# Performance work log

Hardware: AMD Instinct MI355X
Metric: run time of the kernel (lower is better)

## Reference

```python
import jax, jax.numpy as jnp
import numpy as np

SEQ, NSTEPS = 8192, 2048
IDIM, HDIM, NL = 256, 1024, 4


def setup_inputs() -> dict:
    key = jax.random.key(0)
    ks = jax.random.split(key, 6)
    s = 0.02  # small init so tanh recurrence stays well-conditioned
    return {
        "xs": jax.random.normal(ks[0], (SEQ, IDIM), dtype=jnp.float32),
        "Wx0": jax.random.normal(ks[1], (IDIM, HDIM), dtype=jnp.float32) * s,
        "Wh0": jax.random.normal(ks[2], (HDIM, HDIM), dtype=jnp.float32) * s,
        "b0": jnp.zeros((HDIM,), dtype=jnp.float32),
        "Wx_rest": jax.random.normal(ks[3], (NL - 1, HDIM, HDIM), dtype=jnp.float32) * s,
        "Wh_rest": jax.random.normal(ks[4], (NL - 1, HDIM, HDIM), dtype=jnp.float32) * s,
        "b_rest": jnp.zeros((NL - 1, HDIM), dtype=jnp.float32),
        "out_W": jax.random.normal(ks[5], (IDIM, HDIM), dtype=jnp.float32) * s,  # eqx Linear: (out, in)
        "out_b": jnp.zeros((IDIM,), dtype=jnp.float32),
        "n_steps": NSTEPS,
    }


def _layer_scan(xs, Wx, Wh, b):
    # open-loop scan of one tanh RNN cell over the whole sequence
    pre = xs @ Wx + b  # (T, H): hoist input projection out of the scan

    def step(h, p):
        h = jnp.tanh(p + h @ Wh)
        return h, h

    h0 = jnp.zeros((Wh.shape[0],), dtype=xs.dtype)
    last, outs = jax.lax.scan(step, h0, pre)
    return last, outs


def reference(xs, Wx0, Wh0, b0, Wx_rest, Wh_rest, b_rest, out_W, out_b, n_steps):
    # open_loop: run each layer's scan over the full sequence
    states = []
    h, seq = _layer_scan(xs, Wx0, Wh0, b0)
    states.append(h)
    for i in range(Wx_rest.shape[0]):
        h, seq = _layer_scan(seq, Wx_rest[i], Wh_rest[i], b_rest[i])
        states.append(h)
    ol_outs = seq @ out_W.T + out_b  # (T, IDIM) vmap'd out_layer

    def ar_step(carry, _):
        sts, x = carry
        new_sts = []
        h = jnp.tanh(x @ Wx0 + sts[0] @ Wh0 + b0)
        new_sts.append(h)
        x = h
        for i in range(Wx_rest.shape[0]):
            h = jnp.tanh(x @ Wx_rest[i] + sts[i + 1] @ Wh_rest[i] + b_rest[i])
            new_sts.append(h)
            x = h
        x = out_W @ x + out_b
        return (tuple(new_sts), x), x

    carry = (tuple(states), ol_outs[-1])
    _, ar_outs = jax.lax.scan(ar_step, carry, None, length=n_steps)
    return jnp.concatenate([ol_outs, ar_outs], axis=0)  # (T + n_steps, IDIM)
```

## Files before the change

kernel.cpp:

```cpp
#include <hip/hip_runtime.h>
#include <math.h>

#define SEQ    8192
#define NSTEPS 2048
#define NTOT   (SEQ + NSTEPS)
#define IDIM   256
#define HDIM   1024

#define NWG    128
#define TPB    512
#define WPB    8
#define RD     8

typedef unsigned long long u64;

#define WT_FLOATS   (8ull*HDIM*HDIM)
#define BF_FLOAT    WT_FLOATS
#define RING_FLOAT  (WT_FLOATS + HDIM)
#define RING_U64S   (4ull*RD*HDIM)
#define PROG_FLOAT  (RING_FLOAT + 2ull*RING_U64S)


__global__ void k_fuse_w(const float* __restrict__ outW, const float* __restrict__ Wx0,
                         float* __restrict__ ws) {
    int l = blockIdx.x * 256 + threadIdx.x;
    int j = blockIdx.y;
    float acc = 0.f;
    for (int k = 0; k < IDIM; ++k)
        acc += outW[(size_t)k * HDIM + l] * Wx0[(size_t)k * HDIM + j];
    ws[(size_t)j * HDIM + l] = acc;
}

__global__ void k_fuse_b(const float* __restrict__ b0, const float* __restrict__ outb,
                         const float* __restrict__ Wx0, float* __restrict__ ws) {
    int j = blockIdx.x * 256 + threadIdx.x;
    float acc = b0[j];
    for (int k = 0; k < IDIM; ++k)
        acc += outb[k] * Wx0[(size_t)k * HDIM + j];
    ws[BF_FLOAT + j] = acc;
}

__global__ void k_pack(const float* __restrict__ Wh0, const float* __restrict__ Wxr,
                       const float* __restrict__ Whr, float* __restrict__ ws) {
    __shared__ float t[32][33];
    int z = blockIdx.z;
    const float* src; int slot;
    if (z == 0)      { src = Wh0;                                  slot = 1; }
    else if (z <= 3) { src = Wxr + (size_t)(z - 1) * HDIM * HDIM;  slot = 2 * z; }
    else             { src = Whr + (size_t)(z - 4) * HDIM * HDIM;  slot = 2 * (z - 4) + 3; }
    int j0 = blockIdx.x * 32, l0 = blockIdx.y * 32;
    t[threadIdx.y][threadIdx.x] = src[(size_t)(l0 + threadIdx.y) * HDIM + j0 + threadIdx.x];
    __syncthreads();
    float* dst = ws + (size_t)slot * HDIM * HDIM;
    dst[(size_t)(j0 + threadIdx.y) * HDIM + (l0 + threadIdx.x)] = t[threadIdx.x][threadIdx.y];
}

__global__ void k_init(float* __restrict__ ws) {
    int t = blockIdx.x * blockDim.x + threadIdx.x;
    ((u64*)(ws + RING_FLOAT))[t] = 0ull;
    if (t < NWG) ((unsigned*)(ws + PROG_FLOAT))[t] = 0u;
}


__device__ __forceinline__ float wsum(float v) {
#pragma unroll
    for (int off = 32; off > 0; off >>= 1) v += __shfl_xor(v, off, 64);
    return v;
}

__device__ __forceinline__ float ftanh(float x) {
    x = fminf(15.f, fmaxf(-15.f, x));
    float e = __builtin_amdgcn_exp2f(x * 2.8853900817779268f);
    return (e - 1.f) * __builtin_amdgcn_rcpf(e + 1.f);
}

__device__ __forceinline__ void capture8(const u64* slot, unsigned want,
                                         float* dst, int lane, int kbase) {
    unsigned done = 0;
    for (;;) {
        u64 v[8];
#pragma unroll
        for (int k = 0; k < 8; ++k) {
            v[k] = 0;
            if (!(done & (1u << k)))
                v[k] = __hip_atomic_load(slot + lane + 64 * (kbase + k),
                                         __ATOMIC_RELAXED, __HIP_MEMORY_SCOPE_AGENT);
        }
#pragma unroll
        for (int k = 0; k < 8; ++k) {
            if (!(done & (1u << k)) && ((unsigned)(v[k] >> 32) == want)) {
                dst[lane + 64 * (kbase + k)] = __uint_as_float((unsigned)v[k]);
                done |= 1u << k;
            }
        }
        if (__all(done == 0xFFu)) return;
    }
}

__global__ __launch_bounds__(TPB, 1) void k_scan(
    const float* __restrict__ xs, const float* __restrict__ Wx0,
    const float* __restrict__ b0, const float* __restrict__ brest,
    const float* __restrict__ outW, const float* __restrict__ outb,
    float* __restrict__ ws, float* __restrict__ out)
{
    const int lane  = threadIdx.x & 63;
    const int wv    = threadIdx.x >> 6;
    const int layer = blockIdx.x >> 5;
    const int wgl   = blockIdx.x & 31;
    const int jw    = wgl * WPB + wv;
    const int j0    = jw * 4;

    __shared__ float ldsOwn[2][HDIM];
    __shared__ float ldsUp[2][HDIM];

    u64* ring = (u64*)(ws + RING_FLOAT);
    unsigned* prog = (unsigned*)(ws + PROG_FLOAT);
    const int cons = (layer + 1) & 3;

    float A[4][16], B[4][16];
#pragma unroll
    for (int c = 0; c < 4; ++c)
#pragma unroll
        for (int k = 0; k < 16; ++k) {
            A[c][k] = ws[((size_t)(2 * layer) * HDIM + (j0 + c)) * HDIM + lane + 64 * k];
            B[c][k] = ws[((size_t)(2 * layer + 1) * HDIM + (j0 + c)) * HDIM + lane + 64 * k];
        }
    float wx0[4][4];
    if (layer == 0) {
#pragma unroll
        for (int c = 0; c < 4; ++c)
#pragma unroll
            for (int k = 0; k < 4; ++k)
                wx0[c][k] = Wx0[(size_t)(lane + 64 * k) * HDIM + (j0 + c)];
    }
    float ow[16]; float obv = 0.f;
    if (layer == 3) {
#pragma unroll
        for (int k = 0; k < 16; ++k) ow[k] = outW[(size_t)jw * HDIM + lane + 64 * k];
        obv = outb[jw];
    }
    float bb[4], bfc[4];
#pragma unroll
    for (int c = 0; c < 4; ++c) {
        bb[c]  = (layer == 0) ? b0[j0 + c] : brest[(size_t)(layer - 1) * HDIM + j0 + c];
        bfc[c] = (layer == 0) ? ws[BF_FLOAT + j0 + c] : 0.f;
    }

    int minp = 0;

    for (int n = 1; n <= NTOT; ++n) {
        const int par = n & 1;
        const bool xphase = (layer == 0) && (n <= SEQ);

        if (minp < n - 7) {
            for (;;) {
                unsigned pv = __hip_atomic_load(&prog[cons * 32 + (lane & 31)],
                                                __ATOMIC_RELAXED, __HIP_MEMORY_SCOPE_AGENT);
#pragma unroll
                for (int off = 32; off > 0; off >>= 1) {
                    unsigned o = (unsigned)__shfl_xor((int)pv, off, 64);
                    pv = pv < o ? pv : o;
                }
                minp = (int)pv;
                if (minp >= n - 7) break;
                __builtin_amdgcn_s_sleep(2);
            }
        }

        float xv[4];
        if (xphase) {
            const float* xr = xs + (size_t)(n - 1) * IDIM;
#pragma unroll
            for (int k = 0; k < 4; ++k) xv[k] = xr[lane + 64 * k];
        }

        if (wv < 2) {
            capture8(ring + ((size_t)layer * RD + ((n - 1) & (RD - 1))) * HDIM,
                     (unsigned)(n - 1), ldsOwn[par], lane, wv * 8);
        } else if (wv < 4 && !xphase) {
            const int ul = (layer == 0) ? 3 : layer - 1;
            const unsigned want = (layer == 0) ? (unsigned)(n - 1) : (unsigned)n;
            capture8(ring + ((size_t)ul * RD + (want & (RD - 1))) * HDIM,
                     want, ldsUp[par], lane, (wv - 2) * 8);
        }
        __syncthreads();
        if (threadIdx.x == 0)
            __hip_atomic_store(&prog[blockIdx.x], (unsigned)n, __ATOMIC_RELAXED, __HIP_MEMORY_SCOPE_AGENT);

        float a0 = 0.f, a1 = 0.f, a2 = 0.f, a3 = 0.f;
        if (xphase) {
#pragma unroll
            for (int k = 0; k < 4; ++k) {
                float x = xv[k];
                a0 += x * wx0[0][k]; a1 += x * wx0[1][k]; a2 += x * wx0[2][k]; a3 += x * wx0[3][k];
            }
        } else {
#pragma unroll
            for (int k = 0; k < 16; ++k) {
                float x = ldsUp[par][lane + 64 * k];
                a0 += x * A[0][k]; a1 += x * A[1][k]; a2 += x * A[2][k]; a3 += x * A[3][k];
            }
        }
#pragma unroll
        for (int k = 0; k < 16; ++k) {
            float y = ldsOwn[par][lane + 64 * k];
            a0 += y * B[0][k]; a1 += y * B[1][k]; a2 += y * B[2][k]; a3 += y * B[3][k];
        }
        a0 = wsum(a0); a1 = wsum(a1); a2 = wsum(a2); a3 = wsum(a3);
        const bool fph = (layer == 0) && (n > SEQ);
        float r0 = ftanh(a0 + (fph ? bfc[0] : bb[0]));
        float r1 = ftanh(a1 + (fph ? bfc[1] : bb[1]));
        float r2 = ftanh(a2 + (fph ? bfc[2] : bb[2]));
        float r3 = ftanh(a3 + (fph ? bfc[3] : bb[3]));

        {
            u64* dst = ring + ((size_t)layer * RD + (n & (RD - 1))) * HDIM + j0;
            if (lane < 4) {
                float v = (lane == 0) ? r0 : (lane == 1) ? r1 : (lane == 2) ? r2 : r3;
                __hip_atomic_store(dst + lane,
                                   ((u64)(unsigned)n << 32) | (u64)__float_as_uint(v),
                                   __ATOMIC_RELAXED, __HIP_MEMORY_SCOPE_AGENT);
            }
        }

        if (layer == 3 && n >= 2) {
            float a = 0.f;
#pragma unroll
            for (int k = 0; k < 16; ++k) a += ldsOwn[par][lane + 64 * k] * ow[k];
            a = wsum(a);
            if (lane == 0) out[(size_t)(n - 2) * IDIM + jw] = a + obv;
        }
    }

    if (layer == 3) {
        if (wv < 2)
            capture8(ring + ((size_t)3 * RD + (NTOT & (RD - 1))) * HDIM,
                     (unsigned)NTOT, ldsOwn[0], lane, wv * 8);
        __syncthreads();
        float a = 0.f;
#pragma unroll
        for (int k = 0; k < 16; ++k) a += ldsOwn[0][lane + 64 * k] * ow[k];
        a = wsum(a);
        if (lane == 0) out[(size_t)(NTOT - 1) * IDIM + jw] = a + obv;
    }
}


extern "C" void kernel_launch(void* const* d_in, const int* in_sizes, int n_in,
                              void* d_out, int out_size, void* d_ws, size_t ws_size,
                              hipStream_t stream) {
    (void)in_sizes; (void)n_in; (void)out_size; (void)ws_size;
    const float* xs   = (const float*)d_in[0];
    const float* Wx0  = (const float*)d_in[1];
    const float* Wh0  = (const float*)d_in[2];
    const float* b0   = (const float*)d_in[3];
    const float* Wxr  = (const float*)d_in[4];
    const float* Whr  = (const float*)d_in[5];
    const float* brst = (const float*)d_in[6];
    const float* outW = (const float*)d_in[7];
    const float* outb = (const float*)d_in[8];
    float* ws  = (float*)d_ws;
    float* out = (float*)d_out;

    k_fuse_w<<<dim3(4, HDIM), dim3(256), 0, stream>>>(outW, Wx0, ws);
    k_fuse_b<<<dim3(4), dim3(256), 0, stream>>>(b0, outb, Wx0, ws);
    k_pack<<<dim3(32, 32, 7), dim3(32, 32), 0, stream>>>(Wh0, Wxr, Whr, ws);
    k_init<<<dim3(64), dim3(512), 0, stream>>>(ws);

    void* args[] = { (void*)&xs, (void*)&Wx0, (void*)&b0, (void*)&brst,
                     (void*)&outW, (void*)&outb, (void*)&ws, (void*)&out };
    hipError_t e = hipLaunchCooperativeKernel((void*)k_scan, dim3(NWG), dim3(TPB),
                                              args, 0, stream);
    if (e != hipSuccess) {
        k_scan<<<dim3(NWG), dim3(TPB), 0, stream>>>(xs, Wx0, b0, brst, outW, outb, ws, out);
    }
}
```

Measured before the change: 50.00 ms.

## Co-locate each layer's workgroups on one XCD and poll a local-cache ring first

```diff
diff --git a/kernel.cpp b/kernel.cpp
--- a/kernel.cpp
+++ b/kernel.cpp
@@ -7,18 +7,18 @@
 #define IDIM   256
 #define HDIM   1024
 
-#define NWG    128
+#define NWG    256
 #define TPB    512
-#define WPB    8
 #define RD     8
 
 typedef unsigned long long u64;
 
 #define WT_FLOATS   (8ull*HDIM*HDIM)
 #define BF_FLOAT    WT_FLOATS
-#define RING_FLOAT  (WT_FLOATS + HDIM)
-#define RING_U64S   (4ull*RD*HDIM)
-#define PROG_FLOAT  (RING_FLOAT + 2ull*RING_U64S)
+
+__device__ u64 g_llring[4ull * RD * HDIM];
+__device__ u64 g_lring [4ull * RD * HDIM];
+__device__ unsigned g_prog[128];
 
 
 __global__ void k_fuse_w(const float* __restrict__ outW, const float* __restrict__ Wx0,
@@ -55,10 +55,9 @@
     dst[(size_t)(j0 + threadIdx.y) * HDIM + (l0 + threadIdx.x)] = t[threadIdx.x][threadIdx.y];
 }
 
-__global__ void k_init(float* __restrict__ ws) {
-    int t = blockIdx.x * blockDim.x + threadIdx.x;
-    ((u64*)(ws + RING_FLOAT))[t] = 0ull;
-    if (t < NWG) ((unsigned*)(ws + PROG_FLOAT))[t] = 0u;
+__global__ void k_init() {
+    int t = threadIdx.x;
+    if (t < 128) g_prog[t] = 0u;
 }
 
 
@@ -74,27 +73,49 @@
     return (e - 1.f) * __builtin_amdgcn_rcpf(e + 1.f);
 }
 
-__device__ __forceinline__ void capture8(const u64* slot, unsigned want,
-                                         float* dst, int lane, int kbase) {
+__device__ __forceinline__ void ld4_sc0(const u64* p0, const u64* p1,
+                                        const u64* p2, const u64* p3,
+                                        u64& v0, u64& v1, u64& v2, u64& v3) {
+    asm volatile("global_load_dwordx2 %0, %4, off sc0\n\t"
+                 "global_load_dwordx2 %1, %5, off sc0\n\t"
+                 "global_load_dwordx2 %2, %6, off sc0\n\t"
+                 "global_load_dwordx2 %3, %7, off sc0\n\t"
+                 "s_waitcnt vmcnt(0)"
+                 : "=&v"(v0), "=&v"(v1), "=&v"(v2), "=&v"(v3)
+                 : "v"(p0), "v"(p1), "v"(p2), "v"(p3)
+                 : "memory");
+}
+
+__device__ __forceinline__ int cap4_ad(const u64* lb, const u64* gb, unsigned want,
+                                       float* dst, int lane, int kb, int budget) {
+    const int i0 = lane + 64 * (kb + 0), i1 = lane + 64 * (kb + 1);
+    const int i2 = lane + 64 * (kb + 2), i3 = lane + 64 * (kb + 3);
     unsigned done = 0;
+    for (int it = 0; it < budget; ++it) {
+        u64 v0, v1, v2, v3;
+        ld4_sc0(lb + i0, lb + i1, lb + i2, lb + i3, v0, v1, v2, v3);
+        if (!(done & 1u) && (unsigned)(v0 >> 32) == want) { dst[i0] = __uint_as_float((unsigned)v0); done |= 1u; }
+        if (!(done & 2u) && (unsigned)(v1 >> 32) == want) { dst[i1] = __uint_as_float((unsigned)v1); done |= 2u; }
+        if (!(done & 4u) && (unsigned)(v2 >> 32) == want) { dst[i2] = __uint_as_float((unsigned)v2); done |= 4u; }
+        if (!(done & 8u) && (unsigned)(v3 >> 32) == want) { dst[i3] = __uint_as_float((unsigned)v3); done |= 8u; }
+        if (__all(done == 0xFu)) return 1;
+    }
     for (;;) {
-        u64 v[8];
-#pragma unroll
-        for (int k = 0; k < 8; ++k) {
-            v[k] = 0;
-            if (!(done & (1u << k)))
-                v[k] = __hip_atomic_load(slot + lane + 64 * (kbase + k),
-                                         __ATOMIC_RELAXED, __HIP_MEMORY_SCOPE_AGENT);
-        }
-#pragma unroll
-        for (int k = 0; k < 8; ++k) {
-            if (!(done & (1u << k)) && ((unsigned)(v[k] >> 32) == want)) {
-                dst[lane + 64 * (kbase + k)] = __uint_as_float((unsigned)v[k]);
-                done |= 1u << k;
-            }
-        }
-        if (__all(done == 0xFFu)) return;
-    }
+        u64 v0 = __hip_atomic_load(gb + i0, __ATOMIC_RELAXED, __HIP_MEMORY_SCOPE_AGENT);
+        u64 v1 = __hip_atomic_load(gb + i1, __ATOMIC_RELAXED, __HIP_MEMORY_SCOPE_AGENT);
+        u64 v2 = __hip_atomic_load(gb + i2, __ATOMIC_RELAXED, __HIP_MEMORY_SCOPE_AGENT);
+        u64 v3 = __hip_atomic_load(gb + i3, __ATOMIC_RELAXED, __HIP_MEMORY_SCOPE_AGENT);
+        if (!(done & 1u) && (unsigned)(v0 >> 32) == want) { dst[i0] = __uint_as_float((unsigned)v0); done |= 1u; }
+        if (!(done & 2u) && (unsigned)(v1 >> 32) == want) { dst[i1] = __uint_as_float((unsigned)v1); done |= 2u; }
+        if (!(done & 4u) && (unsigned)(v2 >> 32) == want) { dst[i2] = __uint_as_float((unsigned)v2); done |= 4u; }
+        if (!(done & 8u) && (unsigned)(v3 >> 32) == want) { dst[i3] = __uint_as_float((unsigned)v3); done |= 8u; }
+        if (__all(done == 0xFu)) return 0;
+    }
+}
+
+__device__ __forceinline__ void cap4_llc(const u64* gb, unsigned want,
+                                         float* dst, int lane, int kb) {
+    cap4_ad((const u64*)0, gb, want, dst, lane, kb, 0);
 }
 
 __global__ __launch_bounds__(TPB, 1) void k_scan(
@@ -103,19 +124,21 @@
     const float* __restrict__ outW, const float* __restrict__ outb,
     float* __restrict__ ws, float* __restrict__ out)
 {
+    const int res = blockIdx.x & 7;
+    if (res >= 4) return;
+    const int layer = res;
+    const int rank  = blockIdx.x >> 3;
     const int lane  = threadIdx.x & 63;
     const int wv    = threadIdx.x >> 6;
-    const int layer = blockIdx.x >> 5;
-    const int wgl   = blockIdx.x & 31;
-    const int jw    = wgl * WPB + wv;
+    const int jw    = rank * 8 + wv;
     const int j0    = jw * 4;
+    const int cons  = (layer + 1) & 3;
 
     __shared__ float ldsOwn[2][HDIM];
     __shared__ float ldsUp[2][HDIM];
 
-    u64* ring = (u64*)(ws + RING_FLOAT);
-    unsigned* prog = (unsigned*)(ws + PROG_FLOAT);
-    const int cons = (layer + 1) & 3;
+    u64* llr = g_llring + (size_t)layer * RD * HDIM;
+    u64* lr  = g_lring  + (size_t)layer * RD * HDIM;
 
     float A[4][16], B[4][16];
 #pragma unroll
@@ -146,7 +169,14 @@
         bfc[c] = (layer == 0) ? ws[BF_FLOAT + j0 + c] : 0.f;
     }
 
+    if (lane < 4) {
+        __hip_atomic_store(lr + j0 + lane, 0ull, __ATOMIC_RELAXED, __HIP_MEMORY_SCOPE_WORKGROUP);
+        __hip_atomic_store(llr + j0 + lane, 0ull, __ATOMIC_RELAXED, __HIP_MEMORY_SCOPE_AGENT);
+    }
+
     int minp = 0;
+    int local_ok = 1;
+    int miss = 0;
 
     for (int n = 1; n <= NTOT; ++n) {
         const int par = n & 1;
@@ -154,12 +184,12 @@
 
         if (minp < n - 7) {
             for (;;) {
-                unsigned pv = __hip_atomic_load(&prog[cons * 32 + (lane & 31)],
+                unsigned pv = __hip_atomic_load(&g_prog[cons * 32 + (lane & 31)],
                                                 __ATOMIC_RELAXED, __HIP_MEMORY_SCOPE_AGENT);
 #pragma unroll
                 for (int off = 32; off > 0; off >>= 1) {
-                    unsigned o = (unsigned)__shfl_xor((int)pv, off, 64);
-                    pv = pv < o ? pv : o;
+                    unsigned o2 = (unsigned)__shfl_xor((int)pv, off, 64);
+                    pv = pv < o2 ? pv : o2;
                 }
                 minp = (int)pv;
                 if (minp >= n - 7) break;
@@ -174,18 +204,23 @@
             for (int k = 0; k < 4; ++k) xv[k] = xr[lane + 64 * k];
         }
 
-        if (wv < 2) {
-            capture8(ring + ((size_t)layer * RD + ((n - 1) & (RD - 1))) * HDIM,
-                     (unsigned)(n - 1), ldsOwn[par], lane, wv * 8);
-        } else if (wv < 4 && !xphase) {
+        if (wv < 4) {
+            const size_t so = (size_t)((n - 1) & (RD - 1)) * HDIM;
+            int budget = local_ok ? (n <= 2 ? 2000 : 24) : 0;
+            int loc = cap4_ad(lr + so, llr + so, (unsigned)(n - 1),
+                              ldsOwn[par], lane, wv * 4, budget);
+            if (loc) miss = 0;
+            else if (local_ok && ++miss >= 2) local_ok = 0;
+        } else if (!xphase) {
             const int ul = (layer == 0) ? 3 : layer - 1;
             const unsigned want = (layer == 0) ? (unsigned)(n - 1) : (unsigned)n;
-            capture8(ring + ((size_t)ul * RD + (want & (RD - 1))) * HDIM,
-                     want, ldsUp[par], lane, (wv - 2) * 8);
+            const u64* ub = g_llring + ((size_t)ul * RD + (want & (RD - 1))) * HDIM;
+            cap4_llc(ub, want, ldsUp[par], lane, (wv - 4) * 4);
         }
         __syncthreads();
         if (threadIdx.x == 0)
-            __hip_atomic_store(&prog[blockIdx.x], (unsigned)n, __ATOMIC_RELAXED, __HIP_MEMORY_SCOPE_AGENT);
+            __hip_atomic_store(&g_prog[layer * 32 + rank], (unsigned)n,
+                               __ATOMIC_RELAXED, __HIP_MEMORY_SCOPE_AGENT);
 
         float a0 = 0.f, a1 = 0.f, a2 = 0.f, a3 = 0.f;
         if (xphase) {
@@ -214,12 +249,12 @@
         float r3 = ftanh(a3 + (fph ? bfc[3] : bb[3]));
 
         {
-            u64* dst = ring + ((size_t)layer * RD + (n & (RD - 1))) * HDIM + j0;
+            const size_t so = (size_t)(n & (RD - 1)) * HDIM + j0;
             if (lane < 4) {
                 float v = (lane == 0) ? r0 : (lane == 1) ? r1 : (lane == 2) ? r2 : r3;
-                __hip_atomic_store(dst + lane,
-                                   ((u64)(unsigned)n << 32) | (u64)__float_as_uint(v),
-                                   __ATOMIC_RELAXED, __HIP_MEMORY_SCOPE_AGENT);
+                u64 tv = ((u64)(unsigned)n << 32) | (u64)__float_as_uint(v);
+                __hip_atomic_store(lr + so + lane, tv, __ATOMIC_RELAXED, __HIP_MEMORY_SCOPE_WORKGROUP);
+                __hip_atomic_store(llr + so + lane, tv, __ATOMIC_RELAXED, __HIP_MEMORY_SCOPE_AGENT);
             }
         }
 
@@ -233,9 +268,11 @@
     }
 
     if (layer == 3) {
-        if (wv < 2)
-            capture8(ring + ((size_t)3 * RD + (NTOT & (RD - 1))) * HDIM,
-                     (unsigned)NTOT, ldsOwn[0], lane, wv * 8);
+        if (wv < 4) {
+            const size_t so = (size_t)(NTOT & (RD - 1)) * HDIM;
+            cap4_ad(lr + so, llr + so, (unsigned)NTOT, ldsOwn[0], lane, wv * 4,
+                    local_ok ? 2000 : 0);
+        }
         __syncthreads();
         float a = 0.f;
 #pragma unroll
@@ -265,7 +302,7 @@
     k_fuse_w<<<dim3(4, HDIM), dim3(256), 0, stream>>>(outW, Wx0, ws);
     k_fuse_b<<<dim3(4), dim3(256), 0, stream>>>(b0, outb, Wx0, ws);
     k_pack<<<dim3(32, 32, 7), dim3(32, 32), 0, stream>>>(Wh0, Wxr, Whr, ws);
-    k_init<<<dim3(64), dim3(512), 0, stream>>>(ws);
+    k_init<<<dim3(1), dim3(512), 0, stream>>>();
 
     void* args[] = { (void*)&xs, (void*)&Wx0, (void*)&b0, (void*)&brst,
                      (void*)&outW, (void*)&outb, (void*)&ws, (void*)&out };
```

Result: slower. 70.12 ms (+40.2%).

## Move ring to device globals and gate ring polling on per-block publish counters

Applied to the files above, without the earlier changes.

```diff
diff --git a/kernel.cpp b/kernel.cpp
--- a/kernel.cpp
+++ b/kernel.cpp
@@ -16,9 +16,10 @@
 
 #define WT_FLOATS   (8ull*HDIM*HDIM)
 #define BF_FLOAT    WT_FLOATS
-#define RING_FLOAT  (WT_FLOATS + HDIM)
-#define RING_U64S   (4ull*RD*HDIM)
-#define PROG_FLOAT  (RING_FLOAT + 2ull*RING_U64S)
+
+__device__ u64 g_ring[4ull * RD * HDIM];
+__device__ unsigned g_pub[NWG];
+__device__ unsigned g_prog[NWG];
 
 
 __global__ void k_fuse_w(const float* __restrict__ outW, const float* __restrict__ Wx0,
@@ -55,10 +56,9 @@
     dst[(size_t)(j0 + threadIdx.y) * HDIM + (l0 + threadIdx.x)] = t[threadIdx.x][threadIdx.y];
 }
 
-__global__ void k_init(float* __restrict__ ws) {
-    int t = blockIdx.x * blockDim.x + threadIdx.x;
-    ((u64*)(ws + RING_FLOAT))[t] = 0ull;
-    if (t < NWG) ((unsigned*)(ws + PROG_FLOAT))[t] = 0u;
+__global__ void k_init() {
+    int t = threadIdx.x;
+    if (t < NWG) { g_pub[t] = 0u; g_prog[t] = 0u; }
 }
 
 
@@ -74,26 +74,38 @@
     return (e - 1.f) * __builtin_amdgcn_rcpf(e + 1.f);
 }
 
+__device__ __forceinline__ u64 ald(const u64* p) {
+    return __hip_atomic_load(p, __ATOMIC_RELAXED, __HIP_MEMORY_SCOPE_AGENT);
+}
+
 __device__ __forceinline__ void capture8(const u64* slot, unsigned want,
-                                         float* dst, int lane, int kbase) {
+                                         float* dst, int lane, int kb,
+                                         const unsigned* pubg, int gate_after) {
     unsigned done = 0;
-    for (;;) {
+    for (int attempt = 0; ; ++attempt) {
         u64 v[8];
 #pragma unroll
         for (int k = 0; k < 8; ++k) {
             v[k] = 0;
             if (!(done & (1u << k)))
-                v[k] = __hip_atomic_load(slot + lane + 64 * (kbase + k),
-                                         __ATOMIC_RELAXED, __HIP_MEMORY_SCOPE_AGENT);
+                v[k] = ald(slot + lane + 64 * (kb + k));
         }
 #pragma unroll
         for (int k = 0; k < 8; ++k) {
-            if (!(done & (1u << k)) && ((unsigned)(v[k] >> 32) == want)) {
-                dst[lane + 64 * (kbase + k)] = __uint_as_float((unsigned)v[k]);
+            if (!(done & (1u << k)) && (unsigned)(v[k] >> 32) == want) {
+                dst[lane + 64 * (kb + k)] = __uint_as_float((unsigned)v[k]);
                 done |= 1u << k;
             }
         }
         if (__all(done == 0xFFu)) return;
+        if (attempt == gate_after) {
+            for (;;) {
+                unsigned p = (lane < 32)
+                    ? __hip_atomic_load(pubg + lane, __ATOMIC_RELAXED, __HIP_MEMORY_SCOPE_AGENT)
+                    : want;
+                if (__all(p >= want)) break;
+            }
+        }
     }
 }
 
@@ -106,16 +118,13 @@
     const int lane  = threadIdx.x & 63;
     const int wv    = threadIdx.x >> 6;
     const int layer = blockIdx.x >> 5;
-    const int wgl   = blockIdx.x & 31;
-    const int jw    = wgl * WPB + wv;
+    const int rank  = blockIdx.x & 31;
+    const int jw    = rank * 8 + wv;
     const int j0    = jw * 4;
-
-    __shared__ float ldsOwn[2][HDIM];
-    __shared__ float ldsUp[2][HDIM];
-
-    u64* ring = (u64*)(ws + RING_FLOAT);
-    unsigned* prog = (unsigned*)(ws + PROG_FLOAT);
-    const int cons = (layer + 1) & 3;
+    const int cons  = (layer + 1) & 3;
+
+    __shared__ float ldsOwn[HDIM];
+    __shared__ float ldsUp[HDIM];
 
     float A[4][16], B[4][16];
 #pragma unroll
@@ -149,17 +158,16 @@
     int minp = 0;
 
     for (int n = 1; n <= NTOT; ++n) {
-        const int par = n & 1;
         const bool xphase = (layer == 0) && (n <= SEQ);
 
         if (minp < n - 7) {
             for (;;) {
-                unsigned pv = __hip_atomic_load(&prog[cons * 32 + (lane & 31)],
+                unsigned pv = __hip_atomic_load(&g_prog[cons * 32 + (lane & 31)],
                                                 __ATOMIC_RELAXED, __HIP_MEMORY_SCOPE_AGENT);
 #pragma unroll
                 for (int off = 32; off > 0; off >>= 1) {
-                    unsigned o = (unsigned)__shfl_xor((int)pv, off, 64);
-                    pv = pv < o ? pv : o;
+                    unsigned o2 = (unsigned)__shfl_xor((int)pv, off, 64);
+                    pv = pv < o2 ? pv : o2;
                 }
                 minp = (int)pv;
                 if (minp >= n - 7) break;
@@ -175,17 +183,25 @@
         }
 
         if (wv < 2) {
-            capture8(ring + ((size_t)layer * RD + ((n - 1) & (RD - 1))) * HDIM,
-                     (unsigned)(n - 1), ldsOwn[par], lane, wv * 8);
+            if (n == 1) {
+#pragma unroll
+                for (int k = 0; k < 8; ++k) ldsOwn[lane + 64 * (wv * 8 + k)] = 0.f;
+            } else {
+                const u64* sp = g_ring + ((size_t)layer * RD + ((n - 1) & (RD - 1))) * HDIM;
+                capture8(sp, (unsigned)(n - 1), ldsOwn, lane, wv * 8,
+                         g_pub + layer * 32, 4);
+            }
         } else if (wv < 4 && !xphase) {
             const int ul = (layer == 0) ? 3 : layer - 1;
             const unsigned want = (layer == 0) ? (unsigned)(n - 1) : (unsigned)n;
-            capture8(ring + ((size_t)ul * RD + (want & (RD - 1))) * HDIM,
-                     want, ldsUp[par], lane, (wv - 2) * 8);
+            const u64* up = g_ring + ((size_t)ul * RD + (want & (RD - 1))) * HDIM;
+            capture8(up, want, ldsUp, lane, (wv - 2) * 8,
+                     g_pub + ul * 32, 0);
         }
         __syncthreads();
         if (threadIdx.x == 0)
-            __hip_atomic_store(&prog[blockIdx.x], (unsigned)n, __ATOMIC_RELAXED, __HIP_MEMORY_SCOPE_AGENT);
+            __hip_atomic_store(&g_prog[blockIdx.x], (unsigned)n,
+                               __ATOMIC_RELAXED, __HIP_MEMORY_SCOPE_AGENT);
 
         float a0 = 0.f, a1 = 0.f, a2 = 0.f, a3 = 0.f;
         if (xphase) {
@@ -197,13 +213,13 @@
         } else {
 #pragma unroll
             for (int k = 0; k < 16; ++k) {
-                float x = ldsUp[par][lane + 64 * k];
+                float x = ldsUp[lane + 64 * k];
                 a0 += x * A[0][k]; a1 += x * A[1][k]; a2 += x * A[2][k]; a3 += x * A[3][k];
             }
         }
 #pragma unroll
         for (int k = 0; k < 16; ++k) {
-            float y = ldsOwn[par][lane + 64 * k];
+            float y = ldsOwn[lane + 64 * k];
             a0 += y * B[0][k]; a1 += y * B[1][k]; a2 += y * B[2][k]; a3 += y * B[3][k];
         }
         a0 = wsum(a0); a1 = wsum(a1); a2 = wsum(a2); a3 = wsum(a3);
@@ -214,7 +230,7 @@
         float r3 = ftanh(a3 + (fph ? bfc[3] : bb[3]));
 
         {
-            u64* dst = ring + ((size_t)layer * RD + (n & (RD - 1))) * HDIM + j0;
+            u64* dst = g_ring + ((size_t)layer * RD + (n & (RD - 1))) * HDIM + j0;
             if (lane < 4) {
                 float v = (lane == 0) ? r0 : (lane == 1) ? r1 : (lane == 2) ? r2 : r3;
                 __hip_atomic_store(dst + lane,
@@ -226,20 +242,26 @@
         if (layer == 3 && n >= 2) {
             float a = 0.f;
 #pragma unroll
-            for (int k = 0; k < 16; ++k) a += ldsOwn[par][lane + 64 * k] * ow[k];
+            for (int k = 0; k < 16; ++k) a += ldsOwn[lane + 64 * k] * ow[k];
             a = wsum(a);
             if (lane == 0) out[(size_t)(n - 2) * IDIM + jw] = a + obv;
         }
+
+        __syncthreads();
+        if (threadIdx.x == 0)
+            __hip_atomic_store(&g_pub[blockIdx.x], (unsigned)n,
+                               __ATOMIC_RELAXED, __HIP_MEMORY_SCOPE_AGENT);
     }
 
     if (layer == 3) {
-        if (wv < 2)
-            capture8(ring + ((size_t)3 * RD + (NTOT & (RD - 1))) * HDIM,
-                     (unsigned)NTOT, ldsOwn[0], lane, wv * 8);
+        if (wv < 2) {
+            const u64* sp = g_ring + ((size_t)3 * RD + (NTOT & (RD - 1))) * HDIM;
+            capture8(sp, (unsigned)NTOT, ldsOwn, lane, wv * 8, g_pub + 3 * 32, 4);
+        }
         __syncthreads();
         float a = 0.f;
 #pragma unroll
-        for (int k = 0; k < 16; ++k) a += ldsOwn[0][lane + 64 * k] * ow[k];
+        for (int k = 0; k < 16; ++k) a += ldsOwn[lane + 64 * k] * ow[k];
         a = wsum(a);
         if (lane == 0) out[(size_t)(NTOT - 1) * IDIM + jw] = a + obv;
     }
@@ -265,7 +287,7 @@
     k_fuse_w<<<dim3(4, HDIM), dim3(256), 0, stream>>>(outW, Wx0, ws);
     k_fuse_b<<<dim3(4), dim3(256), 0, stream>>>(b0, outb, Wx0, ws);
     k_pack<<<dim3(32, 32, 7), dim3(32, 32), 0, stream>>>(Wh0, Wxr, Whr, ws);
-    k_init<<<dim3(64), dim3(512), 0, stream>>>(ws);
+    k_init<<<dim3(1), dim3(256), 0, stream>>>();
 
     void* args[] = { (void*)&xs, (void*)&Wx0, (void*)&b0, (void*)&brst,
                      (void*)&outW, (void*)&outb, (void*)&ws, (void*)&out };
```

Measured after the change: 58.86 ms. 1.18x slower.
